# Kernel optimization log

Hardware: AMD Instinct MI355X
Metric: run time of the kernel (lower is better)

## Reference

```python
import jax, jax.numpy as jnp
import numpy as np

B, F, NB, E = 32768, 64, 64, 32


def setup_inputs() -> dict:
    key = jax.random.key(0)
    k1, k2, k3, k4 = jax.random.split(key, 4)
    x = jax.random.normal(k1, (B, F), dtype=jnp.float32)
    # per-feature sorted bin edges (as produced by PLE.adapt quantiles)
    bins = jnp.sort(jax.random.uniform(k2, (F, NB), dtype=jnp.float32,
                                       minval=-2.0, maxval=2.0), axis=1)
    W = jax.random.normal(k3, (F, NB, E), dtype=jnp.float32) / np.sqrt(NB)
    b = jax.random.normal(k4, (F, E), dtype=jnp.float32)
    return {"x": x, "bins": bins, "W": W, "b": b}


def reference(x, bins, W, b):
    # x: [B,F], bins: [F,NB] sorted edges, W: [F,NB,E], b: [F,E]
    nb = bins.shape[1]
    lo = bins  # bins[j] == lookup_table[i-1] for bin i=j+1
    # lookup_table.get(i, -1): last bin has no upper edge -> defaults to -1.0
    hi = jnp.concatenate(
        [bins[:, 1:], jnp.full((bins.shape[0], 1), -1.0, bins.dtype)], axis=1)
    j = jnp.arange(nb)
    xe = x[:, :, None]                                  # [B,F,1]
    left = (xe < lo[None]) & (j > 0)                    # [B,F,NB]
    right = (xe >= hi[None]) & (j < nb - 1)             # [B,F,NB]
    v = (xe - lo[None]) / (hi - lo)[None]               # interpolation value
    # enc = 0 where left, 1 where neither, v where exactly one of left/right
    enc = jnp.where(left != right, v, jnp.where(left, 0.0, 1.0))  # [B,F,NB]
    # per-feature linear + ReLU, then features stacked along dim 1
    emb = jax.nn.relu(jnp.einsum('bfn,fne->bfe', enc, W) + b[None])  # [B,F,E]
    return emb
```

## Files before the change

kernel.cpp:

```cpp
#include <hip/hip_runtime.h>


#define FDIM 64
#define NB   64
#define EDIM 32
#define FSL  8
#define NRPB 256
#define ITERS (NRPB / 32)
#define SWSTR 34

typedef __attribute__((ext_vector_type(4))) float f32x4;

static __device__ __forceinline__ unsigned bf16rne(float f) {
    unsigned u = __float_as_uint(f);
    return (u + 0x7FFFu + ((u >> 16) & 1u)) >> 16;
}

__global__ __launch_bounds__(256) void nemb_fused(
    const float* __restrict__ x, const float* __restrict__ bins,
    const float* __restrict__ W, const float* __restrict__ bias,
    float* __restrict__ out)
{
    __shared__ unsigned short sW16[FSL * NB * SWSTR];
    __shared__ float sBins[FSL * 65];
    __shared__ float sP[FSL * EDIM];
    __shared__ float sR[FSL * EDIM];

    const int t     = threadIdx.x;
    const int slice = blockIdx.x & 7;
    const int chunk = blockIdx.x >> 3;
    const int f0    = slice * FSL;

    const int w  = t >> 6;
    const int l  = t & 63;
    const int rs = l >> 3;
    const int fs = l & 7;
    const int ft = l >> 3;
    const int e0 = (l & 7) * 4;

    const long r00 = (long)chunk * NRPB;

    float x_cur  = x[(r00 + w * 8 + rs) * FDIM + f0 + fs];
    float bias_v = bias[(f0 + (t >> 5)) * EDIM + (t & 31)];

    const float* Wg = W + (size_t)f0 * NB * EDIM;
    unsigned* sWd = reinterpret_cast<unsigned*>(sW16);
    #pragma unroll
    for (int i = 0; i < 16; ++i) {
        int qi = i * 256 + t;
        f32x4 v = reinterpret_cast<const f32x4*>(Wg)[qi];
        int gi = qi * 4;
        int fl = gi >> 11;
        int n  = (gi >> 5) & 63;
        int ee = gi & 31;
        unsigned u0 = bf16rne(v.x) | (bf16rne(v.y) << 16);
        unsigned u1 = bf16rne(v.z) | (bf16rne(v.w) << 16);
        int d0 = 17 * (fl * 64 + n) + (ee >> 1);
        sWd[d0]     = u0;
        sWd[d0 + 1] = u1;
    }
    if (t < 128) {
        f32x4 v = reinterpret_cast<const f32x4*>(bins + (size_t)f0 * NB)[t];
        int gi = t * 4;
        int fl = gi >> 6, n = gi & 63;
        float* d = &sBins[fl * 65 + n];
        d[0] = v.x; d[1] = v.y; d[2] = v.z; d[3] = v.w;
    }
    if (t < FSL) sBins[t * 65 + 64] = -1.0f;
    __syncthreads();

    {
        const int fl = t >> 5;
        const int e  = t & 31;
        float p = 0.0f, q = 0.0f;
        #pragma unroll
        for (int n = 0; n < NB; ++n) {
            float lo = sBins[fl * 65 + n];
            float hi = sBins[fl * 65 + n + 1];
            float gv = __builtin_amdgcn_rcpf(hi - lo);
            float wv = __uint_as_float((unsigned)sW16[(fl * 64 + n) * SWSTR + e] << 16);
            p = fmaf(gv, wv, p);
            q = fmaf(lo * gv, wv, q);
        }
        sP[fl * EDIM + e] = p;
        sR[fl * EDIM + e] = bias_v - q;
    }
    __syncthreads();

    const f32x4 Pv = *reinterpret_cast<const f32x4*>(&sP[ft * EDIM + e0]);
    const f32x4 Rv = *reinterpret_cast<const f32x4*>(&sR[ft * EDIM + e0]);

    const float* bl = &sBins[fs * 65];
    const int bp_base = (l >> 3) * 4;

    #pragma unroll 2
    for (int it = 0; it < ITERS; ++it) {
        const long rb = r00 + it * 32 + w * 8;

        float xv = x_cur;
        if (it + 1 < ITERS)
            x_cur = x[(rb + 32 + rs) * FDIM + f0 + fs];

        int k = 0;
        k += (bl[ 8] <= xv) ? 8 : 0;
        k += (bl[16] <= xv) ? 8 : 0;
        k += (bl[24] <= xv) ? 8 : 0;
        k += (bl[32] <= xv) ? 8 : 0;
        k += (bl[40] <= xv) ? 8 : 0;
        k += (bl[48] <= xv) ? 8 : 0;
        k += (bl[56] <= xv) ? 8 : 0;
        {
            const float* b2 = bl + k;
            int inner = 0;
            inner += (b2[1] <= xv) ? 1 : 0;
            inner += (b2[2] <= xv) ? 1 : 0;
            inner += (b2[3] <= xv) ? 1 : 0;
            inner += (b2[4] <= xv) ? 1 : 0;
            inner += (b2[5] <= xv) ? 1 : 0;
            inner += (b2[6] <= xv) ? 1 : 0;
            inner += (b2[7] <= xv) ? 1 : 0;
            k += inner;
        }
        float lo = bl[k];
        float hi = bl[k + 1];
        float cv = (hi - xv) * __builtin_amdgcn_rcpf(hi - lo);

        #pragma unroll
        for (int r = 0; r < 8; ++r) {
            const int a = bp_base + r * 32;
            float xr = __uint_as_float((unsigned)
                __builtin_amdgcn_ds_bpermute(a, (int)__float_as_uint(xv)));
            float cr = __uint_as_float((unsigned)
                __builtin_amdgcn_ds_bpermute(a, (int)__float_as_uint(cv)));
            int   kr = __builtin_amdgcn_ds_bpermute(a, k);

            int d0 = 17 * (ft * 64 + kr) + ((l & 7) << 1);
            unsigned u0 = sWd[d0];
            unsigned u1 = sWd[d0 + 1];
            f32x4 Wv;
            Wv.x = __uint_as_float(u0 << 16);
            Wv.y = __uint_as_float(u0 & 0xFFFF0000u);
            Wv.z = __uint_as_float(u1 << 16);
            Wv.w = __uint_as_float(u1 & 0xFFFF0000u);

            f32x4 o;
            o.x = fmaxf(fmaf(cr, Wv.x, fmaf(xr, Pv.x, Rv.x)), 0.0f);
            o.y = fmaxf(fmaf(cr, Wv.y, fmaf(xr, Pv.y, Rv.y)), 0.0f);
            o.z = fmaxf(fmaf(cr, Wv.z, fmaf(xr, Pv.z, Rv.z)), 0.0f);
            o.w = fmaxf(fmaf(cr, Wv.w, fmaf(xr, Pv.w, Rv.w)), 0.0f);
            *reinterpret_cast<f32x4*>(
                out + (rb + r) * (FDIM * EDIM) + (f0 + ft) * EDIM + e0) = o;
        }
    }
}

extern "C" void kernel_launch(void* const* d_in, const int* in_sizes, int n_in,
                              void* d_out, int out_size, void* d_ws, size_t ws_size,
                              hipStream_t stream) {
    const float* x    = (const float*)d_in[0];
    const float* bins = (const float*)d_in[1];
    const float* W    = (const float*)d_in[2];
    const float* bias = (const float*)d_in[3];
    float* out = (float*)d_out;

    const int B = in_sizes[0] / FDIM;
    const int nchunks = B / NRPB;

    nemb_fused<<<nchunks * 8, 256, 0, stream>>>(x, bins, W, bias, out);
}
```

Before: 56.39 us.

## Widen block feature slice to 16 and halve rows per block

Each block now covers 16 features instead of 8 and 128 rows instead of 256, so each lane handles two feature groups (A and B) per row. The output write per row becomes a 512-float contiguous span, and x loads cover 16 consecutive features. The grid keeps the same block count, but each block converts twice as much W into shared memory (about 70KB LDS), which lowers occupancy and doubles the per-block prologue.

```diff
diff --git a/kernel.cpp b/kernel.cpp
--- a/kernel.cpp
+++ b/kernel.cpp
@@ -4,9 +4,9 @@
 #define FDIM 64
 #define NB   64
 #define EDIM 32
-#define FSL  8
-#define NRPB 256
-#define ITERS (NRPB / 32)
+#define FSL  16
+#define NRPB 128
+#define ITERS (NRPB / 16)
 #define SWSTR 34
 
 typedef __attribute__((ext_vector_type(4))) float f32x4;
@@ -27,26 +27,28 @@
     __shared__ float sR[FSL * EDIM];
 
     const int t     = threadIdx.x;
-    const int slice = blockIdx.x & 7;
-    const int chunk = blockIdx.x >> 3;
+    const int slice = blockIdx.x & 3;
+    const int chunk = blockIdx.x >> 2;
     const int f0    = slice * FSL;
 
-    const int w  = t >> 6;
-    const int l  = t & 63;
-    const int rs = l >> 3;
-    const int fs = l & 7;
-    const int ft = l >> 3;
-    const int e0 = (l & 7) * 4;
+    const int w   = t >> 6;
+    const int l   = t & 63;
+    const int rs  = l >> 4;
+    const int fs  = l & 15;
+    const int ftA = l >> 3;
+    const int ftB = ftA + 8;
+    const int e0  = (l & 7) * 4;
 
     const long r00 = (long)chunk * NRPB;
 
-    float x_cur  = x[(r00 + w * 8 + rs) * FDIM + f0 + fs];
-    float bias_v = bias[(f0 + (t >> 5)) * EDIM + (t & 31)];
+    float x_cur  = x[(r00 + w * 4 + rs) * FDIM + f0 + fs];
+    float biasv0 = bias[(f0 + (t >> 5)) * EDIM + (t & 31)];
+    float biasv1 = bias[(f0 + 8 + (t >> 5)) * EDIM + (t & 31)];
 
     const float* Wg = W + (size_t)f0 * NB * EDIM;
     unsigned* sWd = reinterpret_cast<unsigned*>(sW16);
     #pragma unroll
-    for (int i = 0; i < 16; ++i) {
+    for (int i = 0; i < 32; ++i) {
         int qi = i * 256 + t;
         f32x4 v = reinterpret_cast<const f32x4*>(Wg)[qi];
         int gi = qi * 4;
@@ -59,7 +61,7 @@
         sWd[d0]     = u0;
         sWd[d0 + 1] = u1;
     }
-    if (t < 128) {
+    {
         f32x4 v = reinterpret_cast<const f32x4*>(bins + (size_t)f0 * NB)[t];
         int gi = t * 4;
         int fl = gi >> 6, n = gi & 63;
@@ -69,37 +71,42 @@
     if (t < FSL) sBins[t * 65 + 64] = -1.0f;
     __syncthreads();
 
-    {
-        const int fl = t >> 5;
+    #pragma unroll
+    for (int p = 0; p < 2; ++p) {
+        const int fl = (t >> 5) + p * 8;
         const int e  = t & 31;
-        float p = 0.0f, q = 0.0f;
+        float pp = 0.0f, qq = 0.0f;
         #pragma unroll
         for (int n = 0; n < NB; ++n) {
             float lo = sBins[fl * 65 + n];
             float hi = sBins[fl * 65 + n + 1];
             float gv = __builtin_amdgcn_rcpf(hi - lo);
-            float wv = __uint_as_float((unsigned)sW16[(fl * 64 + n) * SWSTR + e] << 16);
-            p = fmaf(gv, wv, p);
-            q = fmaf(lo * gv, wv, q);
+            float wv = __uint_as_float(
+                (unsigned)sW16[(fl * 64 + n) * SWSTR + e] << 16);
+            pp = fmaf(gv, wv, pp);
+            qq = fmaf(lo * gv, wv, qq);
         }
-        sP[fl * EDIM + e] = p;
-        sR[fl * EDIM + e] = bias_v - q;
+        sP[fl * EDIM + e] = pp;
+        sR[fl * EDIM + e] = (p ? biasv1 : biasv0) - qq;
     }
     __syncthreads();
 
-    const f32x4 Pv = *reinterpret_cast<const f32x4*>(&sP[ft * EDIM + e0]);
-    const f32x4 Rv = *reinterpret_cast<const f32x4*>(&sR[ft * EDIM + e0]);
+    const f32x4 PvA = *reinterpret_cast<const f32x4*>(&sP[ftA * EDIM + e0]);
+    const f32x4 RvA = *reinterpret_cast<const f32x4*>(&sR[ftA * EDIM + e0]);
+    const f32x4 PvB = *reinterpret_cast<const f32x4*>(&sP[ftB * EDIM + e0]);
+    const f32x4 RvB = *reinterpret_cast<const f32x4*>(&sR[ftB * EDIM + e0]);
 
     const float* bl = &sBins[fs * 65];
-    const int bp_base = (l >> 3) * 4;
+    const int aA0 = ftA * 4;
+    const int aB0 = ftB * 4;
 
     #pragma unroll 2
     for (int it = 0; it < ITERS; ++it) {
-        const long rb = r00 + it * 32 + w * 8;
+        const long rb = r00 + it * 16 + w * 4;
 
         float xv = x_cur;
         if (it + 1 < ITERS)
-            x_cur = x[(rb + 32 + rs) * FDIM + f0 + fs];
+            x_cur = x[(rb + 16 + rs) * FDIM + f0 + fs];
 
         int k = 0;
         k += (bl[ 8] <= xv) ? 8 : 0;
@@ -126,30 +133,47 @@
         float cv = (hi - xv) * __builtin_amdgcn_rcpf(hi - lo);
 
         #pragma unroll
-        for (int r = 0; r < 8; ++r) {
-            const int a = bp_base + r * 32;
-            float xr = __uint_as_float((unsigned)
-                __builtin_amdgcn_ds_bpermute(a, (int)__float_as_uint(xv)));
-            float cr = __uint_as_float((unsigned)
-                __builtin_amdgcn_ds_bpermute(a, (int)__float_as_uint(cv)));
-            int   kr = __builtin_amdgcn_ds_bpermute(a, k);
+        for (int r = 0; r < 4; ++r) {
+            const int aA = aA0 + r * 64;
+            const int aB = aB0 + r * 64;
+            float xrA = __uint_as_float((unsigned)
+                __builtin_amdgcn_ds_bpermute(aA, (int)__float_as_uint(xv)));
+            float crA = __uint_as_float((unsigned)
+                __builtin_amdgcn_ds_bpermute(aA, (int)__float_as_uint(cv)));
+            int   krA = __builtin_amdgcn_ds_bpermute(aA, k);
+            float xrB = __uint_as_float((unsigned)
+                __builtin_amdgcn_ds_bpermute(aB, (int)__float_as_uint(xv)));
+            float crB = __uint_as_float((unsigned)
+                __builtin_amdgcn_ds_bpermute(aB, (int)__float_as_uint(cv)));
+            int   krB = __builtin_amdgcn_ds_bpermute(aB, k);
 
-            int d0 = 17 * (ft * 64 + kr) + ((l & 7) << 1);
-            unsigned u0 = sWd[d0];
-            unsigned u1 = sWd[d0 + 1];
-            f32x4 Wv;
-            Wv.x = __uint_as_float(u0 << 16);
-            Wv.y = __uint_as_float(u0 & 0xFFFF0000u);
-            Wv.z = __uint_as_float(u1 << 16);
-            Wv.w = __uint_as_float(u1 & 0xFFFF0000u);
+            int dA = 17 * (ftA * 64 + krA) + ((l & 7) << 1);
+            int dB = 17 * (ftB * 64 + krB) + ((l & 7) << 1);
+            unsigned a0 = sWd[dA], a1 = sWd[dA + 1];
+            unsigned b0 = sWd[dB], b1 = sWd[dB + 1];
+            f32x4 WvA, WvB;
+            WvA.x = __uint_as_float(a0 << 16);
+            WvA.y = __uint_as_float(a0 & 0xFFFF0000u);
+            WvA.z = __uint_as_float(a1 << 16);
+            WvA.w = __uint_as_float(a1 & 0xFFFF0000u);
+            WvB.x = __uint_as_float(b0 << 16);
+            WvB.y = __uint_as_float(b0 & 0xFFFF0000u);
+            WvB.z = __uint_as_float(b1 << 16);
+            WvB.w = __uint_as_float(b1 & 0xFFFF0000u);
 
-            f32x4 o;
-            o.x = fmaxf(fmaf(cr, Wv.x, fmaf(xr, Pv.x, Rv.x)), 0.0f);
-            o.y = fmaxf(fmaf(cr, Wv.y, fmaf(xr, Pv.y, Rv.y)), 0.0f);
-            o.z = fmaxf(fmaf(cr, Wv.z, fmaf(xr, Pv.z, Rv.z)), 0.0f);
-            o.w = fmaxf(fmaf(cr, Wv.w, fmaf(xr, Pv.w, Rv.w)), 0.0f);
-            *reinterpret_cast<f32x4*>(
-                out + (rb + r) * (FDIM * EDIM) + (f0 + ft) * EDIM + e0) = o;
+            f32x4 oA, oB;
+            oA.x = fmaxf(fmaf(crA, WvA.x, fmaf(xrA, PvA.x, RvA.x)), 0.0f);
+            oA.y = fmaxf(fmaf(crA, WvA.y, fmaf(xrA, PvA.y, RvA.y)), 0.0f);
+            oA.z = fmaxf(fmaf(crA, WvA.z, fmaf(xrA, PvA.z, RvA.z)), 0.0f);
+            oA.w = fmaxf(fmaf(crA, WvA.w, fmaf(xrA, PvA.w, RvA.w)), 0.0f);
+            oB.x = fmaxf(fmaf(crB, WvB.x, fmaf(xrB, PvB.x, RvB.x)), 0.0f);
+            oB.y = fmaxf(fmaf(crB, WvB.y, fmaf(xrB, PvB.y, RvB.y)), 0.0f);
+            oB.z = fmaxf(fmaf(crB, WvB.z, fmaf(xrB, PvB.z, RvB.z)), 0.0f);
+            oB.w = fmaxf(fmaf(crB, WvB.w, fmaf(xrB, PvB.w, RvB.w)), 0.0f);
+
+            float* base = out + (rb + r) * (FDIM * EDIM) + f0 * EDIM;
+            *reinterpret_cast<f32x4*>(base + ftA * EDIM + e0) = oA;
+            *reinterpret_cast<f32x4*>(base + ftB * EDIM + e0) = oB;
         }
     }
 }
@@ -166,5 +190,5 @@
     const int B = in_sizes[0] / FDIM;
     const int nchunks = B / NRPB;
 
-    nemb_fused<<<nchunks * 8, 256, 0, stream>>>(x, bins, W, bias, out);
+    nemb_fused<<<nchunks * 4, 256, 0, stream>>>(x, bins, W, bias, out);
 }
```

After: 57.35 us. About the same (+1.7%).
